# Optimization experiments

Measured on AMD Instinct MI355X. Metric: run time of the kernel, lower is better.

The kernel has to match this reference:

```python
import jax, jax.numpy as jnp
import numpy as np

B, P, T = 64, 8400, 100


def _corners(b):
    # b: [..., 4] in (cx, cy, w, h) -> (x1, y1, x2, y2)
    cx, cy, w, h = b[..., 0], b[..., 1], b[..., 2], b[..., 3]
    return cx - w / 2, cy - h / 2, cx + w / 2, cy + h / 2


def _pairwise_iou(pred_box, tgt_box):
    # pred_box: [B, P, 4], tgt_box: [B, T, 4] -> iou [B, T, P]
    px1, py1, px2, py2 = _corners(pred_box[:, None, :, :])   # [B,1,P]
    tx1, ty1, tx2, ty2 = _corners(tgt_box[:, :, None, :])    # [B,T,1]
    ix1 = jnp.maximum(px1, tx1)
    iy1 = jnp.maximum(py1, ty1)
    ix2 = jnp.minimum(px2, tx2)
    iy2 = jnp.minimum(py2, ty2)
    inter = jnp.maximum(ix2 - ix1, 0.0) * jnp.maximum(iy2 - iy1, 0.0)
    area_p = (px2 - px1) * (py2 - py1)
    area_t = (tx2 - tx1) * (ty2 - ty1)
    return inter / (area_p + area_t - inter + 1e-6)


def setup_inputs() -> dict:
    key = jax.random.key(0)
    k1, k2, k3 = jax.random.split(key, 3)
    predictions = jax.random.uniform(k1, (B, P, 5), dtype=jnp.float32)
    targets = jax.random.uniform(k2, (B, T, 5), dtype=jnp.float32)
    lengths = jax.random.randint(k3, (B,), 0, T, dtype=jnp.int64)
    return {"predictions": predictions, "targets": targets, "lengths": lengths}


def reference(predictions, targets, lengths):
    # predictions: [B, P, 5], targets: [B, T, 5], lengths: [B]
    iou = _pairwise_iou(predictions[..., 1:], targets[..., 1:])  # [B, T, P]
    # strict '>' in original keeps first max; argmax also returns first occurrence
    best_idx = jnp.argmax(iou, axis=-1)                          # [B, T]
    matched = jnp.take_along_axis(predictions, best_idx[..., None], axis=1)  # [B, T, 5]
    sq = jnp.sum((matched - targets) ** 2, axis=-1)              # [B, T]
    valid = jnp.arange(targets.shape[1]) < lengths[:, None]      # [B, T]
    loss = jnp.sum(jnp.where(valid, sq, 0.0)) / predictions.shape[0]
    return loss
```

## Files before the change

kernel.cpp:

```cpp
#include <hip/hip_runtime.h>

#define BB 64
#define PP 8400
#define TT 100
#define TG 10
#define NGRP (TT / TG)

__global__ __launch_bounds__(256) void yolo_match_kernel(
    const float* __restrict__ pred,
    const float* __restrict__ tgt,
    const int*   __restrict__ lengths,
    float* __restrict__ ws)
{
#pragma clang fp contract(off)
    const int blk = blockIdx.x;
    const int b   = blk / NGRP;
    const int grp = blk - b * NGRP;
    const int t0  = grp * TG;
    const int tid = threadIdx.x;

    const float* pb = pred + (size_t)b * PP * 5;
    const float* tb = tgt  + ((size_t)b * TT + t0) * 5;

    float tx1[TG], ty1[TG], tx2[TG], ty2[TG], ta[TG];
#pragma unroll
    for (int g = 0; g < TG; ++g) {
        const float tcx = tb[g * 5 + 1], tcy = tb[g * 5 + 2];
        const float tw  = tb[g * 5 + 3], th  = tb[g * 5 + 4];
        tx1[g] = tcx - tw * 0.5f;
        ty1[g] = tcy - th * 0.5f;
        tx2[g] = tcx + tw * 0.5f;
        ty2[g] = tcy + th * 0.5f;
        ta[g]  = (tx2[g] - tx1[g]) * (ty2[g] - ty1[g]);
    }

    float best[TG];
    int   bidx[TG];
#pragma unroll
    for (int g = 0; g < TG; ++g) { best[g] = -1.0f; bidx[g] = 0; }

    for (int p = tid; p < PP; p += 256) {
        const float* bp = pb + p * 5;
        const float cx = bp[1], cy = bp[2], w = bp[3], h = bp[4];
        const float px1 = cx - w * 0.5f;
        const float py1 = cy - h * 0.5f;
        const float px2 = cx + w * 0.5f;
        const float py2 = cy + h * 0.5f;
        const float area_p = (px2 - px1) * (py2 - py1);

#pragma unroll
        for (int g = 0; g < TG; ++g) {
            const float ix1 = fmaxf(px1, tx1[g]);
            const float iy1 = fmaxf(py1, ty1[g]);
            const float ix2 = fminf(px2, tx2[g]);
            const float iy2 = fminf(py2, ty2[g]);
            const float inter = fmaxf(ix2 - ix1, 0.0f) * fmaxf(iy2 - iy1, 0.0f);
            const float denom = ((area_p + ta[g]) - inter) + 1e-6f;
            const float iou   = inter / denom;
            if (iou > best[g]) { best[g] = iou; bidx[g] = p; }
        }
    }

    const int lane = tid & 63;
    const int wid  = tid >> 6;
    __shared__ float s_best[4][TG];
    __shared__ int   s_bidx[4][TG];
    __shared__ float s_sq[TG];

#pragma unroll
    for (int g = 0; g < TG; ++g) {
        float bv = best[g];
        int   bi = bidx[g];
        for (int off = 32; off > 0; off >>= 1) {
            const float ob = __shfl_down(bv, off, 64);
            const int   oi = __shfl_down(bi, off, 64);
            if (ob > bv || (ob == bv && oi < bi)) { bv = ob; bi = oi; }
        }
        if (lane == 0) { s_best[wid][g] = bv; s_bidx[wid][g] = bi; }
    }
    __syncthreads();

    if (tid < TG) {
        const int g = tid;
        float bv = s_best[0][g];
        int   bi = s_bidx[0][g];
#pragma unroll
        for (int w = 1; w < 4; ++w) {
            const float ob = s_best[w][g];
            const int   oi = s_bidx[w][g];
            if (ob > bv || (ob == bv && oi < bi)) { bv = ob; bi = oi; }
        }
        const float* mp = pb + bi * 5;
        const float* tp = tb + g * 5;
        float sq = 0.0f;
        for (int k = 0; k < 5; ++k) {
            const float d = mp[k] - tp[k];
            sq += d * d;
        }
        const bool valid = ((t0 + g) < lengths[b]);
        s_sq[g] = valid ? sq : 0.0f;
    }
    __syncthreads();

    if (tid == 0) {
        float s = 0.0f;
#pragma unroll
        for (int g = 0; g < TG; ++g) s += s_sq[g];
        ws[blk] = s;
    }
}

__global__ __launch_bounds__(256) void yolo_reduce_kernel(
    const float* __restrict__ ws,
    float* __restrict__ out)
{
    const int tid = threadIdx.x;
    float s = 0.0f;
    for (int i = tid; i < BB * NGRP; i += 256) s += ws[i];

    __shared__ float sm[256];
    sm[tid] = s;
    __syncthreads();
    for (int off = 128; off > 0; off >>= 1) {
        if (tid < off) sm[tid] += sm[tid + off];
        __syncthreads();
    }
    if (tid == 0) out[0] = sm[0] / (float)BB;
}

extern "C" void kernel_launch(void* const* d_in, const int* in_sizes, int n_in,
                              void* d_out, int out_size, void* d_ws, size_t ws_size,
                              hipStream_t stream) {
    const float* pred    = (const float*)d_in[0];
    const float* tgt     = (const float*)d_in[1];
    const int*   lengths = (const int*)d_in[2];
    float* out = (float*)d_out;
    float* ws  = (float*)d_ws;

    yolo_match_kernel<<<BB * NGRP, 256, 0, stream>>>(pred, tgt, lengths, ws);
    yolo_reduce_kernel<<<1, 256, 0, stream>>>(ws, out);
}
```

Measured before the change: 121.0 us.

## Vectorize prediction loads as float4, halve target group, swizzle block-to-batch mapping

Each thread now loads four predictions at once as five float4 vectors instead of strided scalar loads, cutting load instructions. The target group size drops from 10 to 5, which doubles the block count to improve occupancy but doubles redundant prediction reads. Block indices are also remapped so that consecutive blocks cover eight different batches, likely to spread work across XCDs and their caches. Each thread handles four predictions per iteration, which increases register pressure.

```diff
diff --git a/kernel.cpp b/kernel.cpp
--- a/kernel.cpp
+++ b/kernel.cpp
@@ -3,7 +3,7 @@
 #define BB 64
 #define PP 8400
 #define TT 100
-#define TG 10
+#define TG 5
 #define NGRP (TT / TG)
 
 __global__ __launch_bounds__(256) void yolo_match_kernel(
@@ -13,14 +13,18 @@
     float* __restrict__ ws)
 {
 #pragma clang fp contract(off)
-    const int blk = blockIdx.x;
-    const int b   = blk / NGRP;
-    const int grp = blk - b * NGRP;
-    const int t0  = grp * TG;
-    const int tid = threadIdx.x;
+    const int blkraw = blockIdx.x;
+    const int x    = blkraw & 7;
+    const int r    = blkraw >> 3;
+    const int bhi  = r / NGRP;
+    const int grp  = r - bhi * NGRP;
+    const int b    = x + 8 * bhi;
+    const int t0   = grp * TG;
+    const int tid  = threadIdx.x;
 
-    const float* pb = pred + (size_t)b * PP * 5;
-    const float* tb = tgt  + ((size_t)b * TT + t0) * 5;
+    const float*  pb  = pred + (size_t)b * PP * 5;
+    const float4* pb4 = (const float4*)pb;
+    const float*  tb  = tgt + ((size_t)b * TT + t0) * 5;
 
     float tx1[TG], ty1[TG], tx2[TG], ty2[TG], ta[TG];
 #pragma unroll
@@ -39,25 +43,37 @@
 #pragma unroll
     for (int g = 0; g < TG; ++g) { best[g] = -1.0f; bidx[g] = 0; }
 
-    for (int p = tid; p < PP; p += 256) {
-        const float* bp = pb + p * 5;
-        const float cx = bp[1], cy = bp[2], w = bp[3], h = bp[4];
-        const float px1 = cx - w * 0.5f;
-        const float py1 = cy - h * 0.5f;
-        const float px2 = cx + w * 0.5f;
-        const float py2 = cy + h * 0.5f;
-        const float area_p = (px2 - px1) * (py2 - py1);
+    for (int g0 = tid; g0 < PP / 4; g0 += 256) {
+        const float4 v0 = pb4[g0 * 5 + 0];
+        const float4 v1 = pb4[g0 * 5 + 1];
+        const float4 v2 = pb4[g0 * 5 + 2];
+        const float4 v3 = pb4[g0 * 5 + 3];
+        const float4 v4 = pb4[g0 * 5 + 4];
+        const float cxs[4] = { v0.y, v1.z, v2.w, v4.x };
+        const float cys[4] = { v0.z, v1.w, v3.x, v4.y };
+        const float wss[4] = { v0.w, v2.x, v3.y, v4.z };
+        const float hss[4] = { v1.x, v2.y, v3.z, v4.w };
 
 #pragma unroll
-        for (int g = 0; g < TG; ++g) {
-            const float ix1 = fmaxf(px1, tx1[g]);
-            const float iy1 = fmaxf(py1, ty1[g]);
-            const float ix2 = fminf(px2, tx2[g]);
-            const float iy2 = fminf(py2, ty2[g]);
-            const float inter = fmaxf(ix2 - ix1, 0.0f) * fmaxf(iy2 - iy1, 0.0f);
-            const float denom = ((area_p + ta[g]) - inter) + 1e-6f;
-            const float iou   = inter / denom;
-            if (iou > best[g]) { best[g] = iou; bidx[g] = p; }
+        for (int j = 0; j < 4; ++j) {
+            const float px1 = cxs[j] - wss[j] * 0.5f;
+            const float py1 = cys[j] - hss[j] * 0.5f;
+            const float px2 = cxs[j] + wss[j] * 0.5f;
+            const float py2 = cys[j] + hss[j] * 0.5f;
+            const float area_p = (px2 - px1) * (py2 - py1);
+            const int   p = g0 * 4 + j;
+
+#pragma unroll
+            for (int g = 0; g < TG; ++g) {
+                const float ix1 = fmaxf(px1, tx1[g]);
+                const float iy1 = fmaxf(py1, ty1[g]);
+                const float ix2 = fminf(px2, tx2[g]);
+                const float iy2 = fminf(py2, ty2[g]);
+                const float inter = fmaxf(ix2 - ix1, 0.0f) * fmaxf(iy2 - iy1, 0.0f);
+                const float denom = ((area_p + ta[g]) - inter) + 1e-6f;
+                const float iou   = inter / denom;
+                if (iou > best[g]) { best[g] = iou; bidx[g] = p; }
+            }
         }
     }
 
@@ -106,7 +122,7 @@
         float s = 0.0f;
 #pragma unroll
         for (int g = 0; g < TG; ++g) s += s_sq[g];
-        ws[blk] = s;
+        ws[blkraw] = s;
     }
 }
 
```

After: 103.5 us. 1.17x faster.
